# Kernel optimization log

Measured on AMD Instinct MI355X. Metric: run time of the kernel, lower is better.

## Reference

```python
import jax, jax.numpy as jnp
import numpy as np

NUM_HEADS = 16
QK_DIM = 64
V_DIM = 64
SCALE = 64 ** (-0.5)  # original_qk_dim ** -0.5


def setup_inputs() -> dict:
    key = jax.random.key(0)
    k1, k2, k3, k4, k5 = jax.random.split(key, 5)
    B, S, D = 4, 2048, 1024
    total_qk = NUM_HEADS * QK_DIM
    total_v = NUM_HEADS * V_DIM
    return {
        "x": jax.random.normal(k1, (B, S, D), jnp.float32),
        "qkv_w": jax.random.normal(k2, (2 * total_qk + total_v, D), jnp.float32) * 0.02,
        "qkv_b": jax.random.normal(k3, (2 * total_qk + total_v,), jnp.float32) * 0.02,
        "proj_w": jax.random.normal(k4, (D, total_v), jnp.float32) * 0.02,
        "proj_b": jax.random.normal(k5, (D,), jnp.float32) * 0.02,
    }


def reference(x, qkv_w, qkv_b, proj_w, proj_b):
    B, S, _ = x.shape
    total_qk = NUM_HEADS * QK_DIM
    total_v = NUM_HEADS * V_DIM
    # fused QKV projection (torch Linear: x @ W^T + b)
    qkv = jnp.einsum('bsd,fd->bsf', x, qkv_w) + qkv_b
    q, k, v = jnp.split(qkv, [total_qk, 2 * total_qk], axis=-1)
    q = q.reshape(B, S, NUM_HEADS, QK_DIM).transpose(0, 2, 1, 3)  # [B,H,S,dk]
    k = k.reshape(B, S, NUM_HEADS, QK_DIM).transpose(0, 2, 1, 3)
    v = v.reshape(B, S, NUM_HEADS, V_DIM).transpose(0, 2, 1, 3)   # [B,H,S,dv]
    scores = jnp.einsum('bhqd,bhkd->bhqk', q, k) * SCALE
    attn = jax.nn.softmax(scores, axis=-1)
    out = jnp.einsum('bhqk,bhkd->bhqd', attn, v)  # [B,H,S,dv]
    out = out.transpose(0, 2, 1, 3).reshape(B, S, total_v)
    return jnp.einsum('bsf,df->bsd', out, proj_w) + proj_b
```

## Files before the change

### kernel.cpp

```cpp
#include <hip/hip_runtime.h>
#include <stdint.h>

typedef float f32x4 __attribute__((ext_vector_type(4)));
typedef short bf16x8 __attribute__((ext_vector_type(8)));
typedef unsigned int u32x4 __attribute__((ext_vector_type(4)));
typedef unsigned short u16;
typedef unsigned int u32;

#define SCL2 0.1803368801111243f

static __device__ __forceinline__ u16 f2bf(float f) {
  union { float f; u32 u; } x; x.f = f;
  return (u16)((x.u + 0x7FFFu + ((x.u >> 16) & 1u)) >> 16);
}

static __device__ __forceinline__ u32 pk2(float lo, float hi) {
  u32 r;
  asm("v_cvt_pk_bf16_f32 %0, %1, %2" : "=v"(r) : "v"(lo), "v"(hi));
  return r;
}

static __device__ __forceinline__ f32x4 mma(bf16x8 a, bf16x8 b, f32x4 c) {
  return __builtin_amdgcn_mfma_f32_16x16x32_bf16(a, b, c, 0, 0, 0);
}

static __device__ __forceinline__ void gl_lds16(const u16* g, u16* l) {
  __builtin_amdgcn_global_load_lds((const __attribute__((address_space(1))) void*)g,
                                   (__attribute__((address_space(3))) void*)l, 16, 0, 0);
}

__global__ __launch_bounds__(256) void cvt_all(const float* __restrict__ x,
                                               const float* __restrict__ w1,
                                               const float* __restrict__ w2,
                                               u16* __restrict__ dst) {
  int i = blockIdx.x * blockDim.x + threadIdx.x;
  int stride = gridDim.x * blockDim.x;
  for (; i < 3145728; i += stride) {
    const float4* src;
    int off;
    if (i < 2097152)      { src = (const float4*)x;  off = i; }
    else if (i < 2883584) { src = (const float4*)w1; off = i - 2097152; }
    else                  { src = (const float4*)w2; off = i - 2883584; }
    float4 v = src[off];
    ushort4 o;
    o.x = f2bf(v.x); o.y = f2bf(v.y); o.z = f2bf(v.z); o.w = f2bf(v.w);
    ((ushort4*)dst)[i] = o;
  }
}

static __device__ __forceinline__ void gemm128(const u16* __restrict__ A,
                                               const u16* __restrict__ Bmat,
                                               u16* lA, u16* lB,
                                               int bm, int bn, f32x4 (&acc)[4][4]) {
  const int t = threadIdx.x;
  const int lane = t & 63, wave = t >> 6;
  const int wr = wave >> 1, wc = wave & 1;
  const int g = lane >> 4, r16 = lane & 15;
  const int sw = r16 & 7;
  const int srow = wave * 8 + (lane >> 3);
  const int scol = ((lane & 7) ^ (lane >> 3)) * 8;
  const u16* As = A + (bm + srow) * 1024 + scol;
  const u16* Bs = Bmat + (bn + srow) * 1024 + scol;
  u16* const dA = lA + wave * 512;
  u16* const dB = lB + wave * 512;

  for (int kt = 0; kt < 1024; kt += 64) {
    __syncthreads();
    #pragma unroll
    for (int i = 0; i < 4; i++) {
      gl_lds16(As + kt + i * 32768, dA + i * 2048);
      gl_lds16(Bs + kt + i * 32768, dB + i * 2048);
    }
    __syncthreads();
    #pragma unroll
    for (int kk = 0; kk < 2; kk++) {
      bf16x8 af[4], bfr[4];
      #pragma unroll
      for (int mi = 0; mi < 4; mi++)
        af[mi] = *(const bf16x8*)(lA + (wr * 64 + mi * 16 + r16) * 64 + (((kk * 4 + g) ^ sw) * 8));
      #pragma unroll
      for (int nj = 0; nj < 4; nj++)
        bfr[nj] = *(const bf16x8*)(lB + (wc * 64 + nj * 16 + r16) * 64 + (((kk * 4 + g) ^ sw) * 8));
      #pragma unroll
      for (int mi = 0; mi < 4; mi++)
        #pragma unroll
        for (int nj = 0; nj < 4; nj++)
          acc[mi][nj] = mma(af[mi], bfr[nj], acc[mi][nj]);
    }
  }
}

__global__ __launch_bounds__(256) void k_gemm_qkv(const u16* __restrict__ xb,
                                                  const u16* __restrict__ wb,
                                                  const float* __restrict__ qkv_b,
                                                  u16* __restrict__ Qs,
                                                  u16* __restrict__ Ks,
                                                  u16* __restrict__ Vt) {
  __shared__ __align__(16) u16 lds[18432];
  f32x4 acc[4][4] = {};
  int bid = blockIdx.y * 64 + blockIdx.x;
  int xcd = bid & 7, i0 = bid >> 3;
  int bx = (xcd >> 1) * 16 + i0 / 12;
  int by = (xcd & 1) * 12 + i0 % 12;
  const int bm = bx * 128, bn = by * 128;
  gemm128(xb, wb, lds, lds + 8192, bm, bn, acc);
  const int t = threadIdx.x, lane = t & 63, wave = t >> 6;
  const int wr = wave >> 1, wc = wave & 1;
  const int g = lane >> 4, r16 = lane & 15;
  if (bn < 2048) {
    #pragma unroll
    for (int nj = 0; nj < 4; nj++) {
      int f = bn + wc * 64 + nj * 16 + r16;
      float bias = qkv_b[f];
      int which = f >> 10;
      int fl = f & 1023;
      int h = fl >> 6, dd = fl & 63;
      u16* base = which ? Ks : Qs;
      float scl = which ? 1.f : SCL2;
      #pragma unroll
      for (int mi = 0; mi < 4; mi++) {
        int mb = bm + wr * 64 + mi * 16 + g * 4;
        #pragma unroll
        for (int rg = 0; rg < 4; rg++) {
          int m = mb + rg;
          int b = m >> 11, s = m & 2047;
          base[(((b * 16 + h) * 2048) + s) * 64 + dd] = f2bf((acc[mi][nj][rg] + bias) * scl);
        }
      }
    }
  } else {
    __syncthreads();
    #pragma unroll
    for (int nj = 0; nj < 4; nj++) {
      int fl = wc * 64 + nj * 16 + r16;
      float bias = qkv_b[bn + fl];
      #pragma unroll
      for (int mi = 0; mi < 4; mi++) {
        int ml = wr * 64 + mi * 16 + g * 4;
        *(u32*)(lds + fl * 144 + ml)     = pk2(acc[mi][nj][0] + bias, acc[mi][nj][1] + bias);
        *(u32*)(lds + fl * 144 + ml + 2) = pk2(acc[mi][nj][2] + bias, acc[mi][nj][3] + bias);
      }
    }
    __syncthreads();
    int b = bm >> 11, s0 = bm & 2047;
    #pragma unroll
    for (int i = 0; i < 8; i++) {
      int fl = i * 16 + (t >> 4);
      int m8 = (t & 15) * 8;
      uint4 val = *(uint4*)(lds + fl * 144 + m8);
      int f = bn + fl - 2048;
      int h = f >> 6, dd = f & 63;
      *(uint4*)(Vt + (((b * 16 + h) * 64) + dd) * 2048 + s0 + m8) = val;
    }
  }
}

__global__ __launch_bounds__(256, 4) void k_attn(const u16* __restrict__ Qs,
                                                 const u16* __restrict__ Ks,
                                                 const u16* __restrict__ Vt,
                                                 u16* __restrict__ ctx) {
  __shared__ __align__(16) u16 lKs[2][64 * 64];
  __shared__ __align__(16) u16 lVs[2][64 * 72];
  int bid = blockIdx.x;
  int lin = (bid & 7) * 128 + (bid >> 3);
  const int bh = lin >> 4, qt = lin & 15;
  const int b = bh >> 4, h = bh & 15;
  const u16* Qb = Qs + bh * (2048 * 64);
  const u16* Kb = Ks + bh * (2048 * 64);
  const u16* Vb = Vt + bh * (64 * 2048);
  const int t = threadIdx.x, lane = t & 63, wave = t >> 6;
  const int g = lane >> 4, r16 = lane & 15;
  const int q0 = qt * 128 + wave * 32;

  bf16x8 qf[2][2];
  #pragma unroll
  for (int j = 0; j < 2; j++)
    #pragma unroll
    for (int kk = 0; kk < 2; kk++)
      qf[j][kk] = *(const bf16x8*)(Qb + (q0 + j * 16 + r16) * 64 + kk * 32 + g * 8);

  u32x4 onesw;
  onesw.x = 0x3F803F80u; onesw.y = 0x3F803F80u; onesw.z = 0x3F803F80u; onesw.w = 0x3F803F80u;
  const bf16x8 ones = __builtin_bit_cast(bf16x8, onesw);

  f32x4 o[2][4] = {};
  f32x4 lsum[2] = {};
  const f32x4 INIT4 = {-4.f, -4.f, -4.f, -4.f};

  int kOffG[2], kOffL[2], vOffG[2], vOffL[2];
  #pragma unroll
  for (int i = 0; i < 2; i++) {
    int ci = i * 256 + t;
    int rK = ci >> 3, cK = ci & 7;
    kOffG[i] = rK * 64 + cK * 8;
    kOffL[i] = rK * 64 + ((cK ^ (rK & 7)) * 8);
    int rV = ci >> 3, c8 = ci & 7;
    int kb = c8 >> 2, cc = c8 & 3;
    vOffG[i] = rV * 2048 + c8 * 8;
    vOffL[i] = rV * 72 + kb * 32 + 16 * (cc & 1) + 4 * (cc >> 1);
  }

  uint4 gk[2], gv[2];
  #pragma unroll
  for (int i = 0; i < 2; i++) gk[i] = *(const uint4*)(Kb + kOffG[i]);
  #pragma unroll
  for (int i = 0; i < 2; i++) gv[i] = *(const uint4*)(Vb + vOffG[i]);
  #pragma unroll
  for (int i = 0; i < 2; i++) *(uint4*)(&lKs[0][kOffL[i]]) = gk[i];
  #pragma unroll
  for (int i = 0; i < 2; i++) {
    uint2 lo; lo.x = gv[i].x; lo.y = gv[i].y;
    uint2 hi; hi.x = gv[i].z; hi.y = gv[i].w;
    *(uint2*)(&lVs[0][vOffL[i]]) = lo;
    *(uint2*)(&lVs[0][vOffL[i] + 8]) = hi;
  }
  __syncthreads();

  for (int tt = 0; tt < 32; ++tt) {
    const u16* lKc = lKs[tt & 1];
    const u16* lVc = lVs[tt & 1];
    if (tt < 31) {
      #pragma unroll
      for (int i = 0; i < 2; i++) gk[i] = *(const uint4*)(Kb + (tt + 1) * 4096 + kOffG[i]);
      #pragma unroll
      for (int i = 0; i < 2; i++) gv[i] = *(const uint4*)(Vb + (tt + 1) * 64 + vOffG[i]);
    }
    __builtin_amdgcn_s_setprio(1);
    #pragma unroll
    for (int kb = 0; kb < 2; kb++) {
      const int sw = r16 & 7;
      const u16* kp0 = lKc + (kb * 32 + r16) * 64;
      const u16* kp1 = lKc + (kb * 32 + 16 + r16) * 64;
      bf16x8 kf00 = *(const bf16x8*)(kp0 + ((g ^ sw) * 8));
      bf16x8 kf01 = *(const bf16x8*)(kp0 + (((4 + g) ^ sw) * 8));
      bf16x8 kf10 = *(const bf16x8*)(kp1 + ((g ^ sw) * 8));
      bf16x8 kf11 = *(const bf16x8*)(kp1 + (((4 + g) ^ sw) * 8));
      bf16x8 vf[4];
      #pragma unroll
      for (int tdv = 0; tdv < 4; tdv++)
        vf[tdv] = *(const bf16x8*)(lVc + (tdv * 16 + r16) * 72 + kb * 32 + g * 8);
      #pragma unroll
      for (int j = 0; j < 2; j++) {
        f32x4 z0 = mma(kf00, qf[j][0], INIT4);
        z0 = mma(kf01, qf[j][1], z0);
        f32x4 z1 = mma(kf10, qf[j][0], INIT4);
        z1 = mma(kf11, qf[j][1], z1);
        float e0 = __builtin_amdgcn_exp2f(z0[0]), e1 = __builtin_amdgcn_exp2f(z0[1]);
        float e2 = __builtin_amdgcn_exp2f(z0[2]), e3 = __builtin_amdgcn_exp2f(z0[3]);
        float e4 = __builtin_amdgcn_exp2f(z1[0]), e5 = __builtin_amdgcn_exp2f(z1[1]);
        float e6 = __builtin_amdgcn_exp2f(z1[2]), e7 = __builtin_amdgcn_exp2f(z1[3]);
        u32x4 w_;
        w_.x = pk2(e0, e1); w_.y = pk2(e2, e3);
        w_.z = pk2(e4, e5); w_.w = pk2(e6, e7);
        bf16x8 pa = __builtin_bit_cast(bf16x8, w_);
        #pragma unroll
        for (int tdv = 0; tdv < 4; tdv++)
          o[j][tdv] = mma(pa, vf[tdv], o[j][tdv]);
        lsum[j] = mma(pa, ones, lsum[j]);
      }
    }
    __builtin_amdgcn_s_setprio(0);
    if (tt < 31) {
      u16* lKn = lKs[(tt + 1) & 1];
      u16* lVn = lVs[(tt + 1) & 1];
      #pragma unroll
      for (int i = 0; i < 2; i++) *(uint4*)(&lKn[kOffL[i]]) = gk[i];
      #pragma unroll
      for (int i = 0; i < 2; i++) {
        uint2 lo; lo.x = gv[i].x; lo.y = gv[i].y;
        uint2 hi; hi.x = gv[i].z; hi.y = gv[i].w;
        *(uint2*)(&lVn[vOffL[i]]) = lo;
        *(uint2*)(&lVn[vOffL[i] + 8]) = hi;
      }
    }
    __syncthreads();
  }

  #pragma unroll
  for (int j = 0; j < 2; j++) {
    f32x4 li;
    #pragma unroll
    for (int rg = 0; rg < 4; rg++) li[rg] = 1.0f / lsum[j][rg];
    #pragma unroll
    for (int tdv = 0; tdv < 4; tdv++)
      #pragma unroll
      for (int rg = 0; rg < 4; rg++) {
        int s = q0 + j * 16 + g * 4 + rg;
        ctx[((b * 2048 + s) * 1024) + h * 64 + tdv * 16 + r16] = f2bf(o[j][tdv][rg] * li[rg]);
      }
  }
}

__global__ __launch_bounds__(256) void k_gemm_proj(const u16* __restrict__ ctx,
                                                   const u16* __restrict__ pwb,
                                                   const float* __restrict__ pb,
                                                   float* __restrict__ out) {
  __shared__ __align__(16) u16 lds[16384];
  f32x4 acc[4][4] = {};
  int bid = blockIdx.y * 64 + blockIdx.x;
  int xcd = bid & 7, i0 = bid >> 3;
  int bx = xcd * 8 + (i0 >> 3);
  int by = i0 & 7;
  const int bm = bx * 128, bn = by * 128;
  gemm128(ctx, pwb, lds, lds + 8192, bm, bn, acc);
  const int lane = threadIdx.x & 63, wave = threadIdx.x >> 6;
  const int wr = wave >> 1, wc = wave & 1;
  const int g = lane >> 4, r16 = lane & 15;
  #pragma unroll
  for (int nj = 0; nj < 4; nj++) {
    int col = bn + wc * 64 + nj * 16 + r16;
    float bias = pb[col];
    #pragma unroll
    for (int mi = 0; mi < 4; mi++) {
      int mb = bm + wr * 64 + mi * 16 + g * 4;
      #pragma unroll
      for (int rg = 0; rg < 4; rg++)
        out[(mb + rg) * 1024 + col] = acc[mi][nj][rg] + bias;
    }
  }
}

extern "C" void kernel_launch(void* const* d_in, const int* in_sizes, int n_in,
                              void* d_out, int out_size, void* d_ws, size_t ws_size,
                              hipStream_t stream) {
  const float* x      = (const float*)d_in[0];
  const float* qkv_w  = (const float*)d_in[1];
  const float* qkv_b  = (const float*)d_in[2];
  const float* proj_w = (const float*)d_in[3];
  const float* proj_b = (const float*)d_in[4];
  float* out = (float*)d_out;
  char* ws = (char*)d_ws;

  u16* xb  = (u16*)(ws);
  u16* wb  = (u16*)(ws + 16777216);
  u16* pwb = (u16*)(ws + 23068672);
  u16* Qs  = (u16*)(ws + 25165824);
  u16* Ks  = (u16*)(ws + 41943040);
  u16* Vt  = (u16*)(ws + 58720256);
  u16* ctx = (u16*)(ws + 75497472);

  cvt_all<<<2048, 256, 0, stream>>>(x, qkv_w, proj_w, (u16*)ws);
  k_gemm_qkv<<<dim3(64, 24), 256, 0, stream>>>(xb, wb, qkv_b, Qs, Ks, Vt);
  k_attn<<<1024, 256, 0, stream>>>(Qs, Ks, Vt, ctx);
  k_gemm_proj<<<dim3(64, 8), 256, 0, stream>>>(ctx, pwb, proj_b, out);
}
```

Before: 171.8 us.

## Pre-swizzle V in QKV epilogue and load K/V directly global-to-LDS

The QKV projection epilogue now writes V in a per-64-key tiled layout that is already XOR-swizzled. Each attention tile is then a contiguous 4096-element block that can be copied straight into LDS. The attention kernel replaces register-staged global loads and LDS stores for K and V with direct global-to-LDS copies (gl_lds16), removing VGPR staging and the separate LDS store phase. The V LDS read path switches from a padded stride of 72 to a swizzled stride of 64. The risk is that correctness depends on the async copies finishing before the barrier, and the scattered 8-byte V stores in the epilogue may be less efficient.

New measurement: 166.1 us. 3.4% less time.

```diff
diff --git a/kernel.cpp b/kernel.cpp
--- a/kernel.cpp
+++ b/kernel.cpp
@@ -149,8 +149,18 @@
       int m8 = (t & 15) * 8;
       uint4 val = *(uint4*)(lds + fl * 144 + m8);
       int f = bn + fl - 2048;
-      int h = f >> 6, dd = f & 63;
-      *(uint4*)(Vt + (((b * 16 + h) * 64) + dd) * 2048 + s0 + m8) = val;
+      int hd = f >> 6, dv = f & 63;
+      int bh2 = b * 16 + hd;
+      int K0 = s0 + m8;
+      int tt = K0 >> 6, key64 = K0 & 63;
+      int kb2 = key64 >> 5, o = key64 & 31;
+      int ph = o >> 4;
+      int a0 = (o & 15) >> 2;
+      int base2 = ((bh2 * 32 + tt) * 64 + dv) * 64 + 4 * ph;
+      uint2 lo; lo.x = val.x; lo.y = val.y;
+      uint2 hi; hi.x = val.z; hi.y = val.w;
+      *(uint2*)(Vt + base2 + (((kb2 * 4 + a0)     ^ (dv & 7)) * 8)) = lo;
+      *(uint2*)(Vt + base2 + (((kb2 * 4 + a0 + 1) ^ (dv & 7)) * 8)) = hi;
     }
   }
 }
@@ -159,15 +169,15 @@
                                                  const u16* __restrict__ Ks,
                                                  const u16* __restrict__ Vt,
                                                  u16* __restrict__ ctx) {
-  __shared__ __align__(16) u16 lKs[2][64 * 64];
-  __shared__ __align__(16) u16 lVs[2][64 * 72];
+  __shared__ __align__(16) u16 lKs[2][4096];
+  __shared__ __align__(16) u16 lVs[2][4096];
   int bid = blockIdx.x;
   int lin = (bid & 7) * 128 + (bid >> 3);
   const int bh = lin >> 4, qt = lin & 15;
   const int b = bh >> 4, h = bh & 15;
   const u16* Qb = Qs + bh * (2048 * 64);
   const u16* Kb = Ks + bh * (2048 * 64);
-  const u16* Vb = Vt + bh * (64 * 2048);
+  const u16* Vb = Vt + bh * (32 * 4096);
   const int t = threadIdx.x, lane = t & 63, wave = t >> 6;
   const int g = lane >> 4, r16 = lane & 15;
   const int q0 = qt * 128 + wave * 32;
@@ -187,32 +197,20 @@
   f32x4 lsum[2] = {};
   const f32x4 INIT4 = {-4.f, -4.f, -4.f, -4.f};
 
-  int kOffG[2], kOffL[2], vOffG[2], vOffL[2];
+  int kSrc[2], vSrc[2], dOff[2];
   #pragma unroll
   for (int i = 0; i < 2; i++) {
     int ci = i * 256 + t;
-    int rK = ci >> 3, cK = ci & 7;
-    kOffG[i] = rK * 64 + cK * 8;
-    kOffL[i] = rK * 64 + ((cK ^ (rK & 7)) * 8);
-    int rV = ci >> 3, c8 = ci & 7;
-    int kb = c8 >> 2, cc = c8 & 3;
-    vOffG[i] = rV * 2048 + c8 * 8;
-    vOffL[i] = rV * 72 + kb * 32 + 16 * (cc & 1) + 4 * (cc >> 1);
-  }
-
-  uint4 gk[2], gv[2];
-  #pragma unroll
-  for (int i = 0; i < 2; i++) gk[i] = *(const uint4*)(Kb + kOffG[i]);
-  #pragma unroll
-  for (int i = 0; i < 2; i++) gv[i] = *(const uint4*)(Vb + vOffG[i]);
-  #pragma unroll
-  for (int i = 0; i < 2; i++) *(uint4*)(&lKs[0][kOffL[i]]) = gk[i];
+    int rK = ci >> 3, c8 = ci & 7;
+    kSrc[i] = rK * 64 + ((c8 ^ (rK & 7)) * 8);
+    vSrc[i] = ci * 8;
+    dOff[i] = i * 2048 + wave * 512;
+  }
+
   #pragma unroll
   for (int i = 0; i < 2; i++) {
-    uint2 lo; lo.x = gv[i].x; lo.y = gv[i].y;
-    uint2 hi; hi.x = gv[i].z; hi.y = gv[i].w;
-    *(uint2*)(&lVs[0][vOffL[i]]) = lo;
-    *(uint2*)(&lVs[0][vOffL[i] + 8]) = hi;
+    gl_lds16(Kb + kSrc[i], &lKs[0][dOff[i]]);
+    gl_lds16(Vb + vSrc[i], &lVs[0][dOff[i]]);
   }
   __syncthreads();
 
@@ -220,10 +218,15 @@
     const u16* lKc = lKs[tt & 1];
     const u16* lVc = lVs[tt & 1];
     if (tt < 31) {
-      #pragma unroll
-      for (int i = 0; i < 2; i++) gk[i] = *(const uint4*)(Kb + (tt + 1) * 4096 + kOffG[i]);
-      #pragma unroll
-      for (int i = 0; i < 2; i++) gv[i] = *(const uint4*)(Vb + (tt + 1) * 64 + vOffG[i]);
+      const u16* Ksrc = Kb + (tt + 1) * 4096;
+      const u16* Vsrc = Vb + (tt + 1) * 4096;
+      u16* dK = lKs[(tt + 1) & 1];
+      u16* dV = lVs[(tt + 1) & 1];
+      #pragma unroll
+      for (int i = 0; i < 2; i++) {
+        gl_lds16(Ksrc + kSrc[i], dK + dOff[i]);
+        gl_lds16(Vsrc + vSrc[i], dV + dOff[i]);
+      }
     }
     __builtin_amdgcn_s_setprio(1);
     #pragma unroll
@@ -238,7 +241,7 @@
       bf16x8 vf[4];
       #pragma unroll
       for (int tdv = 0; tdv < 4; tdv++)
-        vf[tdv] = *(const bf16x8*)(lVc + (tdv * 16 + r16) * 72 + kb * 32 + g * 8);
+        vf[tdv] = *(const bf16x8*)(lVc + (tdv * 16 + r16) * 64 + (((kb * 4 + g) ^ sw) * 8));
       #pragma unroll
       for (int j = 0; j < 2; j++) {
         f32x4 z0 = mma(kf00, qf[j][0], INIT4);
@@ -260,19 +263,6 @@
       }
     }
     __builtin_amdgcn_s_setprio(0);
-    if (tt < 31) {
-      u16* lKn = lKs[(tt + 1) & 1];
-      u16* lVn = lVs[(tt + 1) & 1];
-      #pragma unroll
-      for (int i = 0; i < 2; i++) *(uint4*)(&lKn[kOffL[i]]) = gk[i];
-      #pragma unroll
-      for (int i = 0; i < 2; i++) {
-        uint2 lo; lo.x = gv[i].x; lo.y = gv[i].y;
-        uint2 hi; hi.x = gv[i].z; hi.y = gv[i].w;
-        *(uint2*)(&lVn[vOffL[i]]) = lo;
-        *(uint2*)(&lVn[vOffL[i] + 8]) = hi;
-      }
-    }
     __syncthreads();
   }
 
```
